# Kernel optimization log

Hardware: AMD Instinct MI355X
Metric: run time of the kernel (lower is better)

## Reference

```python
import jax, jax.numpy as jnp
import numpy as np

STEPS = 8
TOL = 1e-6


def _kabsch(p, q):
    # p, q: [B, N, 3]; returns R [B,3,3], t [B,3] s.t. q ~= R p + t (pypose svdtf)
    pm = p.mean(axis=-2, keepdims=True)
    qm = q.mean(axis=-2, keepdims=True)
    pc = p - pm
    qc = q - qm
    H = jnp.einsum('bni,bnj->bij', pc, qc)          # 3x3 cross-covariance
    U, S, Vt = jnp.linalg.svd(H, full_matrices=False)
    V = jnp.swapaxes(Vt, -1, -2)
    Ut = jnp.swapaxes(U, -1, -2)
    d = jnp.linalg.det(jnp.matmul(V, Ut))            # reflection fix
    D = jnp.concatenate([jnp.ones(d.shape + (2,), d.dtype), d[..., None]], axis=-1)
    R = jnp.matmul(V * D[..., None, :], Ut)
    t = qm[..., 0, :] - jnp.einsum('bij,bj->bi', R, pm[..., 0, :])
    return R, t


def _rotmat_to_quat(R):
    # branchless rotation-matrix -> quaternion [qx, qy, qz, qw] (pypose order)
    r00, r11, r22 = R[..., 0, 0], R[..., 1, 1], R[..., 2, 2]
    qw = 0.5 * jnp.sqrt(jnp.clip(1.0 + r00 + r11 + r22, 1e-12))
    qx = 0.5 * jnp.sqrt(jnp.clip(1.0 + r00 - r11 - r22, 1e-12))
    qy = 0.5 * jnp.sqrt(jnp.clip(1.0 - r00 + r11 - r22, 1e-12))
    qz = 0.5 * jnp.sqrt(jnp.clip(1.0 - r00 - r11 + r22, 1e-12))
    qx = qx * jnp.where(R[..., 2, 1] - R[..., 1, 2] >= 0, 1.0, -1.0)
    qy = qy * jnp.where(R[..., 0, 2] - R[..., 2, 0] >= 0, 1.0, -1.0)
    qz = qz * jnp.where(R[..., 1, 0] - R[..., 0, 1] >= 0, 1.0, -1.0)
    return jnp.stack([qx, qy, qz, qw], axis=-1)


def _icp(psrc, ptgt):
    B = psrc.shape[0]
    tn = (ptgt * ptgt).sum(-1)                        # [B, M]

    def body(carry, _):
        pc, err, done = carry
        # brute-force 1-NN: Euclidean cdist via  |p|^2 + |q|^2 - 2 p.q
        sq = ((pc * pc).sum(-1)[:, :, None] + tn[:, None, :]
              - 2.0 * jnp.einsum('bnd,bmd->bnm', pc, ptgt))
        dist = jnp.sqrt(jnp.clip(sq, 0.0))            # [B, N, M]
        knnd = dist.min(axis=-1)                      # [B, N]
        idx = dist.argmin(axis=-1)                    # [B, N]
        errnew = knnd.mean(axis=-1)                   # [B]
        conv = jnp.all(jnp.abs(errnew - err) < TOL)
        done_new = jnp.logical_or(done, conv)
        qk = jnp.take_along_axis(ptgt, jnp.broadcast_to(idx[..., None], pc.shape), axis=1)
        R, t = _kabsch(pc, qk)
        pcnew = jnp.einsum('bij,bnj->bni', R, pc) + t[:, None, :]
        pc = jnp.where(done_new, pc, pcnew)
        err = jnp.where(done_new, err, errnew)
        return (pc, err, done_new), None

    init = (psrc, jnp.zeros((B,), psrc.dtype), jnp.array(False))
    (pc, _, _), _ = jax.lax.scan(body, init, None, length=STEPS)
    R, t = _kabsch(psrc, pc)                          # final fit psrc -> moved cloud
    quat = _rotmat_to_quat(R)
    return jnp.concatenate([t, quat], axis=-1)        # SE3 7-vector [t, qx,qy,qz,qw]


def setup_inputs() -> dict:
    key = jax.random.key(0)
    k1, k2 = jax.random.split(key)
    psrc = jax.random.normal(k1, (2, 4096, 3), dtype=jnp.float32)
    ptgt = jax.random.normal(k2, (2, 4096, 3), dtype=jnp.float32)
    return {"psrc": psrc, "ptgt": ptgt}


def reference(psrc, ptgt):
    return _icp(psrc, ptgt)
```

## Files before the change

### kernel.cpp

```cpp
#include <hip/hip_runtime.h>
#include <math.h>

#define NPTS 4096
#define MPTS 4096
#define NSTEPS 8
#define ICP_TOL 1e-6f
#define NBLK 256
#define NSUB 16

#define ACC_OFF 32768
#define CTR_OFF 98304
#define CTR_STRIDE 1536
#define STPUB_OFF 110592

__global__ void init_kernel(const float* __restrict__ ptgt, float* __restrict__ ws) {
    float* ptgt4 = ws;
    unsigned* ctrs = (unsigned*)(ws + CTR_OFF);
    int gid = blockIdx.x * 256 + threadIdx.x;
    if (gid < 2 * MPTS) {
        float x = ptgt[3 * gid + 0];
        float y = ptgt[3 * gid + 1];
        float z = ptgt[3 * gid + 2];
        float4 v;
        v.x = x; v.y = y; v.z = z;
        v.w = 0.5f * (x * x + y * y + z * z);
        ((float4*)ptgt4)[gid] = v;
    }
    for (int i = gid; i < NSTEPS * CTR_STRIDE; i += 8192) ctrs[i] = 0u;
}

__device__ __forceinline__ float frcp(float x) {
#if __has_builtin(__builtin_amdgcn_rcpf)
    return __builtin_amdgcn_rcpf(x);
#else
    return 1.f / x;
#endif
}
__device__ __forceinline__ float frsq(float x) {
#if __has_builtin(__builtin_amdgcn_rsqf)
    return __builtin_amdgcn_rsqf(x);
#else
    return 1.f / sqrtf(x);
#endif
}

#define DET3(a,b,c,d,e,f,g,h,i) \
    ((a)*((e)*(i)-(f)*(h)) - (b)*((d)*(i)-(f)*(g)) + (c)*((d)*(h)-(e)*(g)))

__device__ __forceinline__ void horn_quat(const float N[4][4], float q[4]) {
    float s = 1e-30f;
#pragma unroll
    for (int i = 0; i < 4; ++i)
#pragma unroll
        for (int j = 0; j < 4; ++j) s = fmaxf(s, fabsf(N[i][j]));
    float inv = frcp(s);
    float A[4][4], B[4][4];
#pragma unroll
    for (int i = 0; i < 4; ++i)
#pragma unroll
        for (int j = 0; j < 4; ++j) A[i][j] = N[i][j] * inv;
#pragma unroll
    for (int i = 0; i < 4; ++i)
#pragma unroll
        for (int j = i; j < 4; ++j) {
            float v = A[i][0]*A[0][j] + A[i][1]*A[1][j] + A[i][2]*A[2][j] + A[i][3]*A[3][j];
            B[i][j] = v; B[j][i] = v;
        }
    float p1 = A[0][0]+A[1][1]+A[2][2]+A[3][3];
    float p2 = B[0][0]+B[1][1]+B[2][2]+B[3][3];
    float p3 = 0.f, p4 = 0.f;
#pragma unroll
    for (int i = 0; i < 4; ++i)
#pragma unroll
        for (int j = 0; j < 4; ++j) { p3 += A[i][j]*B[i][j]; p4 += B[i][j]*B[i][j]; }
    float e1 = p1;
    float e2 = 0.5f*(e1*p1 - p2);
    float e3 = (e2*p1 - e1*p2 + p3)*(1.f/3.f);
    float e4 = 0.25f*(e3*p1 - e2*p2 + e1*p3 - p4);
    float lam = -3e38f;
#pragma unroll
    for (int i = 0; i < 4; ++i) {
        float r = A[i][i];
#pragma unroll
        for (int j = 0; j < 4; ++j) if (j != i) r += fabsf(A[i][j]);
        lam = fmaxf(lam, r);
    }
#pragma unroll
    for (int it = 0; it < 12; ++it) {
        float pv = (((lam - e1)*lam + e2)*lam - e3)*lam + e4;
        float dv = ((4.f*lam - 3.f*e1)*lam + 2.f*e2)*lam - e3;
        lam -= pv * frcp(dv);
    }
    float M[4][4];
#pragma unroll
    for (int i = 0; i < 4; ++i)
#pragma unroll
        for (int j = 0; j < 4; ++j) M[i][j] = A[i][j] - ((i == j) ? lam : 0.f);
    float C0 = DET3(M[1][1],M[1][2],M[1][3], M[2][1],M[2][2],M[2][3], M[3][1],M[3][2],M[3][3]);
    float C1 = DET3(M[0][0],M[0][2],M[0][3], M[2][0],M[2][2],M[2][3], M[3][0],M[3][2],M[3][3]);
    float C2 = DET3(M[0][0],M[0][1],M[0][3], M[1][0],M[1][1],M[1][3], M[3][0],M[3][1],M[3][3]);
    float C3 = DET3(M[0][0],M[0][1],M[0][2], M[1][0],M[1][1],M[1][2], M[2][0],M[2][1],M[2][2]);
    int is = 0; float cb = fabsf(C0);
    if (fabsf(C1) > cb) { cb = fabsf(C1); is = 1; }
    if (fabsf(C2) > cb) { cb = fabsf(C2); is = 2; }
    if (fabsf(C3) > cb) { cb = fabsf(C3); is = 3; }
    float v0, v1, v2, v3;
#define ROWCOF(a,b,c) { \
    v0 =  DET3(M[a][1],M[a][2],M[a][3], M[b][1],M[b][2],M[b][3], M[c][1],M[c][2],M[c][3]); \
    v1 = -DET3(M[a][0],M[a][2],M[a][3], M[b][0],M[b][2],M[b][3], M[c][0],M[c][2],M[c][3]); \
    v2 =  DET3(M[a][0],M[a][1],M[a][3], M[b][0],M[b][1],M[b][3], M[c][0],M[c][1],M[c][3]); \
    v3 = -DET3(M[a][0],M[a][1],M[a][2], M[b][0],M[b][1],M[b][2], M[c][0],M[c][1],M[c][2]); }
    if (is == 0)      ROWCOF(1,2,3)
    else if (is == 1) ROWCOF(0,2,3)
    else if (is == 2) ROWCOF(0,1,3)
    else              ROWCOF(0,1,2)
#undef ROWCOF
    float nr = frsq(v0*v0 + v1*v1 + v2*v2 + v3*v3);
    q[0] = v0*nr; q[1] = v1*nr; q[2] = v2*nr; q[3] = v3*nr;
}

#define FOR16(OP) OP(0) OP(1) OP(2) OP(3) OP(4) OP(5) OP(6) OP(7) \
                  OP(8) OP(9) OP(10) OP(11) OP(12) OP(13) OP(14) OP(15)

__global__ __launch_bounds__(512, 2) void icp_main(
    const float* __restrict__ psrc, float* __restrict__ ws,
    float* __restrict__ out) {

    float* ptgt4 = ws;
    float* acc = ws + ACC_OFF;
    unsigned* ctrs = (unsigned*)(ws + CTR_OFF);
    float* stpub = ws + STPUB_OFF;

    __shared__ float tshx[MPTS];
    __shared__ float tshy[MPTS];
    __shared__ float tshz[MPTS];
    __shared__ float st[2][13];
    __shared__ unsigned keys[8][16];
    __shared__ float red[16][16];
    __shared__ float gred[2][16][16];
    __shared__ float asum[2][16];
    __shared__ int contflag;

    const int tid = threadIdx.x;
    const int bid = blockIdx.x;
    const int b = bid >> 7;
    const int n0 = (bid & 127) * 32;

    {
        const float4* tp4 = (const float4*)ptgt4 + (size_t)b * MPTS;
        for (int i = tid; i < MPTS; i += 512) {
            float4 v = tp4[i];
            tshx[i] = v.x; tshy[i] = v.y; tshz[i] = v.z;
        }
    }
    if (tid < 2) {
        st[tid][0] = 1.f; st[tid][1] = 0.f; st[tid][2] = 0.f;
        st[tid][3] = 0.f; st[tid][4] = 1.f; st[tid][5] = 0.f;
        st[tid][6] = 0.f; st[tid][7] = 0.f; st[tid][8] = 1.f;
        st[tid][9] = 0.f; st[tid][10] = 0.f; st[tid][11] = 0.f;
        st[tid][12] = 0.f;
    }
    __syncthreads();

    const int w = tid >> 6, lane = tid & 63;
    const int m0 = w * 512 + lane;

    for (int step = 0; step < NSTEPS; ++step) {
        float R00 = st[b][0], R01 = st[b][1], R02 = st[b][2];
        float R10 = st[b][3], R11 = st[b][4], R12 = st[b][5];
        float R20 = st[b][6], R21 = st[b][7], R22 = st[b][8];
        float t0 = st[b][9], t1 = st[b][10], t2 = st[b][11];

        float sacc = 0.f;

        for (int p = 0; p < 2; ++p) {
            const int np = n0 + p * 16;
            const float* ps = psrc + ((size_t)b * NPTS + np) * 3;

#define DECLP(i) float px##i, py##i, pz##i;
            FOR16(DECLP)
#undef DECLP
#define LOADP(i) { float x = ps[3*(i)], y = ps[3*(i)+1], z = ps[3*(i)+2]; \
            px##i = fmaf(R00, x, fmaf(R01, y, fmaf(R02, z, t0))); \
            py##i = fmaf(R10, x, fmaf(R11, y, fmaf(R12, z, t1))); \
            pz##i = fmaf(R20, x, fmaf(R21, y, fmaf(R22, z, t2))); }
            FOR16(LOADP)
#undef LOADP

#define DECLB(i) float bs##i = -3.0e38f; int ix##i = m0;
            FOR16(DECLB)
#undef DECLB

            float tcx = tshx[m0], tcy = tshy[m0], tcz = tshz[m0];
            int mreg = m0;
#pragma unroll
            for (int k = 0; k < 8; ++k) {
                int mn = m0 + ((k + 1) & 7) * 64;
                float tnx = tshx[mn], tny = tshy[mn], tnz = tshz[mn];
                float htn = 0.5f * (tcx * tcx + tcy * tcy + tcz * tcz);
                float tx = tcx, ty = tcy, tz = tcz;
#define PAIR(i) { float s = fmaf(px##i, tx, fmaf(py##i, ty, fmaf(pz##i, tz, -htn))); \
                if (s > bs##i) { bs##i = s; ix##i = mreg; } }
                FOR16(PAIR)
#undef PAIR
                mreg += 64;
                tcx = tnx; tcy = tny; tcz = tnz;
            }

#define REDKEY(i) { unsigned ub = __float_as_uint(bs##i); \
            unsigned u = ((int)ub >= 0) ? (ub | 0x80000000u) : ~ub; \
            unsigned key = (u & 0xFFFFF000u) | (4095u - (unsigned)ix##i); \
            for (int off = 32; off; off >>= 1) { \
                unsigned o = (unsigned)__shfl_xor((int)key, off); \
                key = key > o ? key : o; } \
            if (lane == 0) keys[w][i] = key; }
            FOR16(REDKEY)
#undef REDKEY
            __syncthreads();

            if (tid < 16) {
                unsigned key = keys[0][tid];
#pragma unroll
                for (int ww = 1; ww < 8; ++ww) {
                    unsigned o = keys[ww][tid];
                    key = key > o ? key : o;
                }
                int m = 4095 - (int)(key & 0xFFFu);
                float qx2 = tshx[m], qy2 = tshy[m], qz2 = tshz[m];
                const float* pp = psrc + ((size_t)b * NPTS + np + tid) * 3;
                float x = pp[0], y = pp[1], z = pp[2];
                float px = fmaf(R00, x, fmaf(R01, y, fmaf(R02, z, t0)));
                float py = fmaf(R10, x, fmaf(R11, y, fmaf(R12, z, t1)));
                float pz = fmaf(R20, x, fmaf(R21, y, fmaf(R22, z, t2)));
                float dx = px - qx2, dy = py - qy2, dz = pz - qz2;
                float dist = sqrtf(dx * dx + dy * dy + dz * dz);
                red[tid][0] = px; red[tid][1] = py; red[tid][2] = pz;
                red[tid][3] = qx2; red[tid][4] = qy2; red[tid][5] = qz2;
                red[tid][6] = px * qx2;  red[tid][7] = px * qy2;  red[tid][8] = px * qz2;
                red[tid][9] = py * qx2;  red[tid][10] = py * qy2; red[tid][11] = py * qz2;
                red[tid][12] = pz * qx2; red[tid][13] = pz * qy2; red[tid][14] = pz * qz2;
                red[tid][15] = dist;
            }
            __syncthreads();
            if (tid < 16) {
                float s = 0.f;
#pragma unroll
                for (int r = 0; r < 16; ++r) s += red[r][tid];
                sacc += s;
            }
            __syncthreads();
        }

        if (tid < 16) {
            __hip_atomic_store(&acc[((size_t)step * NBLK + bid) * 16 + tid], sacc,
                               __ATOMIC_RELAXED, __HIP_MEMORY_SCOPE_AGENT);
        }

        unsigned* stepc = ctrs + step * CTR_STRIDE;
        __syncthreads();
        if (tid == 0) {
            unsigned* sub = stepc + (bid & (NSUB - 1)) * 16;
            unsigned old = __hip_atomic_fetch_add(sub, 1u, __ATOMIC_RELAXED,
                                                  __HIP_MEMORY_SCOPE_AGENT);
            if (old == (unsigned)(NBLK / NSUB) - 1u)
                __hip_atomic_fetch_add(stepc + 512, 1u, __ATOMIC_RELAXED,
                                       __HIP_MEMORY_SCOPE_AGENT);
        }

        if (bid == 0) {
            if (tid == 0) {
                while (__hip_atomic_load(stepc + 512, __ATOMIC_RELAXED,
                                         __HIP_MEMORY_SCOPE_AGENT) < (unsigned)NSUB) {
                    __builtin_amdgcn_s_sleep(1);
                }
            }
            __syncthreads();
            {
                const float* accs = acc + (size_t)step * NBLK * 16;
                int bb = tid >> 8;
                int rem = tid & 255;
                int c = rem & 15, g = rem >> 4;
                float ssum = 0.f;
#pragma unroll
                for (int i = 0; i < 8; ++i)
                    ssum += accs[(size_t)(bb * 128 + g * 8 + i) * 16 + c];
                gred[bb][g][c] = ssum;
            }
            __syncthreads();
            if (tid < 32) {
                int bb = tid >> 4, c = tid & 15;
                float s = 0.f;
#pragma unroll
                for (int g = 0; g < 16; ++g) s += gred[bb][g][c];
                asum[bb][c] = s;
            }
            __syncthreads();
            if (tid == 0) {
                float err0 = asum[0][15] * (1.f / NPTS);
                float err1 = asum[1][15] * (1.f / NPTS);
                bool conv = (fabsf(err0 - st[0][12]) < ICP_TOL) &&
                            (fabsf(err1 - st[1][12]) < ICP_TOL);
                contflag = conv ? 2 : 1;
            }
            __syncthreads();
            if (contflag == 1 && tid < 2) {
                float a[16];
                for (int i = 0; i < 16; ++i) a[i] = asum[tid][i];
                const float inv_n = 1.f / NPTS;
                float pmx = a[0]*inv_n, pmy = a[1]*inv_n, pmz = a[2]*inv_n;
                float qmx = a[3]*inv_n, qmy = a[4]*inv_n, qmz = a[5]*inv_n;
                float H[3][3];
                for (int i = 0; i < 3; ++i)
                    for (int j = 0; j < 3; ++j)
                        H[i][j] = a[6 + 3*i + j] - a[i]*a[3 + j]*inv_n;
                float Sxx=H[0][0], Sxy=H[0][1], Sxz=H[0][2];
                float Syx=H[1][0], Syy=H[1][1], Syz=H[1][2];
                float Szx=H[2][0], Szy=H[2][1], Szz=H[2][2];
                float Nm[4][4];
                Nm[0][0] = Sxx+Syy+Szz; Nm[0][1] = Syz-Szy;
                Nm[0][2] = Szx-Sxz;     Nm[0][3] = Sxy-Syx;
                Nm[1][1] = Sxx-Syy-Szz; Nm[1][2] = Sxy+Syx; Nm[1][3] = Szx+Sxz;
                Nm[2][2] = -Sxx+Syy-Szz; Nm[2][3] = Syz+Szy;
                Nm[3][3] = -Sxx-Syy+Szz;
                Nm[1][0]=Nm[0][1]; Nm[2][0]=Nm[0][2]; Nm[3][0]=Nm[0][3];
                Nm[2][1]=Nm[1][2]; Nm[3][1]=Nm[1][3]; Nm[3][2]=Nm[2][3];
                float qv[4];
                horn_quat(Nm, qv);
                float qw = qv[0], qx = qv[1], qy = qv[2], qz = qv[3];
                float R00n = 1.f - 2.f*(qy*qy + qz*qz);
                float R01n = 2.f*(qx*qy - qw*qz);
                float R02n = 2.f*(qx*qz + qw*qy);
                float R10n = 2.f*(qx*qy + qw*qz);
                float R11n = 1.f - 2.f*(qx*qx + qz*qz);
                float R12n = 2.f*(qy*qz - qw*qx);
                float R20n = 2.f*(qx*qz - qw*qy);
                float R21n = 2.f*(qy*qz + qw*qx);
                float R22n = 1.f - 2.f*(qx*qx + qy*qy);
                float tx = qmx - (R00n*pmx + R01n*pmy + R02n*pmz);
                float ty = qmy - (R10n*pmx + R11n*pmy + R12n*pmz);
                float tz = qmz - (R20n*pmx + R21n*pmy + R22n*pmz);
                float C00=st[tid][0], C01=st[tid][1], C02=st[tid][2];
                float C10=st[tid][3], C11=st[tid][4], C12=st[tid][5];
                float C20=st[tid][6], C21=st[tid][7], C22=st[tid][8];
                float T0=st[tid][9], T1=st[tid][10], T2=st[tid][11];
                float ns[12];
                ns[0] = R00n*C00 + R01n*C10 + R02n*C20;
                ns[1] = R00n*C01 + R01n*C11 + R02n*C21;
                ns[2] = R00n*C02 + R01n*C12 + R02n*C22;
                ns[3] = R10n*C00 + R11n*C10 + R12n*C20;
                ns[4] = R10n*C01 + R11n*C11 + R12n*C21;
                ns[5] = R10n*C02 + R11n*C12 + R12n*C22;
                ns[6] = R20n*C00 + R21n*C10 + R22n*C20;
                ns[7] = R20n*C01 + R21n*C11 + R22n*C21;
                ns[8] = R20n*C02 + R21n*C12 + R22n*C22;
                ns[9]  = R00n*T0 + R01n*T1 + R02n*T2 + tx;
                ns[10] = R10n*T0 + R11n*T1 + R12n*T2 + ty;
                ns[11] = R20n*T0 + R21n*T1 + R22n*T2 + tz;
                for (int i = 0; i < 12; ++i) {
                    st[tid][i] = ns[i];
                    __hip_atomic_store(&stpub[step*32 + tid*16 + i], ns[i],
                                       __ATOMIC_RELAXED, __HIP_MEMORY_SCOPE_AGENT);
                }
                st[tid][12] = asum[tid][15] * (1.f / NPTS);
            }
            __syncthreads();
            if (tid == 0) {
                unsigned fv = (unsigned)contflag;
#pragma unroll
                for (int f = 0; f < NSUB; ++f)
                    __hip_atomic_store(stepc + 1024 + f*16, fv,
                                       __ATOMIC_RELAXED, __HIP_MEMORY_SCOPE_AGENT);
            }
            __syncthreads();
        } else {
            if (tid == 0) {
                unsigned* myflag = stepc + 1024 + (bid & (NSUB - 1)) * 16;
                unsigned fv;
                while ((fv = __hip_atomic_load(myflag, __ATOMIC_RELAXED,
                                               __HIP_MEMORY_SCOPE_AGENT)) == 0u) {
                    __builtin_amdgcn_s_sleep(2);
                }
                contflag = (int)fv;
                if (fv == 1u) {
                    for (int i = 0; i < 12; ++i)
                        st[b][i] = __hip_atomic_load(&stpub[step*32 + b*16 + i],
                                                     __ATOMIC_RELAXED,
                                                     __HIP_MEMORY_SCOPE_AGENT);
                }
            }
            __syncthreads();
        }
        if (contflag == 2) break;
    }

    if (bid == 0 && tid < 2) {
        float r00 = st[tid][0], r01 = st[tid][1], r02 = st[tid][2];
        float r10 = st[tid][3], r11 = st[tid][4], r12 = st[tid][5];
        float r20 = st[tid][6], r21 = st[tid][7], r22 = st[tid][8];
        float qw = 0.5f * sqrtf(fmaxf(1.f + r00 + r11 + r22, 1e-12f));
        float qx = 0.5f * sqrtf(fmaxf(1.f + r00 - r11 - r22, 1e-12f));
        float qy = 0.5f * sqrtf(fmaxf(1.f - r00 + r11 - r22, 1e-12f));
        float qz = 0.5f * sqrtf(fmaxf(1.f - r00 - r11 + r22, 1e-12f));
        qx = (r21 - r12 >= 0.f) ? qx : -qx;
        qy = (r02 - r20 >= 0.f) ? qy : -qy;
        qz = (r10 - r01 >= 0.f) ? qz : -qz;
        out[tid * 7 + 0] = st[tid][9];
        out[tid * 7 + 1] = st[tid][10];
        out[tid * 7 + 2] = st[tid][11];
        out[tid * 7 + 3] = qx;
        out[tid * 7 + 4] = qy;
        out[tid * 7 + 5] = qz;
        out[tid * 7 + 6] = qw;
    }
}

extern "C" void kernel_launch(void* const* d_in, const int* in_sizes, int n_in,
                              void* d_out, int out_size, void* d_ws, size_t ws_size,
                              hipStream_t stream) {
    const float* psrc = (const float*)d_in[0];
    const float* ptgt = (const float*)d_in[1];
    float* out = (float*)d_out;
    float* ws = (float*)d_ws;

    init_kernel<<<32, 256, 0, stream>>>(ptgt, ws);
    icp_main<<<NBLK, 512, 0, stream>>>(psrc, ws, out);
}
```

Before: 194.6 us.

## Split grid barrier per batch with two masters and cache source points in LDS

Replaces the single global master block with one master per batch element (blocks 0 and 128). Each master reduces only its own 128 block partials with a vectorized float4 load and a transposed LDS reduction, then computes that batch's Kabsch update in parallel with the other master. The masters exchange convergence flags so both batches still stop together. Source points are cached in shared memory instead of being re-read from global every step. This shortens the serial tail at each step barrier, at the cost of a second cross-block flag handshake that every block must wait on.

Result: faster. 189.2 us (-2.8%).

```diff
diff --git a/kernel.cpp b/kernel.cpp
--- a/kernel.cpp
+++ b/kernel.cpp
@@ -6,11 +6,10 @@
 #define NSTEPS 8
 #define ICP_TOL 1e-6f
 #define NBLK 256
-#define NSUB 16
 
 #define ACC_OFF 32768
 #define CTR_OFF 98304
-#define CTR_STRIDE 1536
+#define CTR_STRIDE 1024
 #define STPUB_OFF 110592
 
 __global__ void init_kernel(const float* __restrict__ ptgt, float* __restrict__ ws) {
@@ -134,12 +133,15 @@
     __shared__ float tshx[MPTS];
     __shared__ float tshy[MPTS];
     __shared__ float tshz[MPTS];
-    __shared__ float st[2][13];
+    __shared__ float spx[32], spy[32], spz[32];
+    __shared__ float stq[13];
     __shared__ unsigned keys[8][16];
     __shared__ float red[16][16];
-    __shared__ float gred[2][16][16];
-    __shared__ float asum[2][16];
-    __shared__ int contflag;
+    __shared__ float gd[16][132];
+    __shared__ float gp[4][16];
+    __shared__ float asum[16];
+    __shared__ float stv[12];
+    __shared__ int fvs[2];
 
     const int tid = threadIdx.x;
     const int bid = blockIdx.x;
@@ -153,34 +155,38 @@
             tshx[i] = v.x; tshy[i] = v.y; tshz[i] = v.z;
         }
     }
-    if (tid < 2) {
-        st[tid][0] = 1.f; st[tid][1] = 0.f; st[tid][2] = 0.f;
-        st[tid][3] = 0.f; st[tid][4] = 1.f; st[tid][5] = 0.f;
-        st[tid][6] = 0.f; st[tid][7] = 0.f; st[tid][8] = 1.f;
-        st[tid][9] = 0.f; st[tid][10] = 0.f; st[tid][11] = 0.f;
-        st[tid][12] = 0.f;
+    if (tid < 32) {
+        const float* pp = psrc + ((size_t)b * NPTS + n0 + tid) * 3;
+        spx[tid] = pp[0]; spy[tid] = pp[1]; spz[tid] = pp[2];
+    }
+    if (tid == 0) {
+        stq[0] = 1.f; stq[1] = 0.f; stq[2] = 0.f;
+        stq[3] = 0.f; stq[4] = 1.f; stq[5] = 0.f;
+        stq[6] = 0.f; stq[7] = 0.f; stq[8] = 1.f;
+        stq[9] = 0.f; stq[10] = 0.f; stq[11] = 0.f;
+        stq[12] = 0.f;
     }
     __syncthreads();
 
     const int w = tid >> 6, lane = tid & 63;
     const int m0 = w * 512 + lane;
+    bool done = false;
 
     for (int step = 0; step < NSTEPS; ++step) {
-        float R00 = st[b][0], R01 = st[b][1], R02 = st[b][2];
-        float R10 = st[b][3], R11 = st[b][4], R12 = st[b][5];
-        float R20 = st[b][6], R21 = st[b][7], R22 = st[b][8];
-        float t0 = st[b][9], t1 = st[b][10], t2 = st[b][11];
+        float R00 = stq[0], R01 = stq[1], R02 = stq[2];
+        float R10 = stq[3], R11 = stq[4], R12 = stq[5];
+        float R20 = stq[6], R21 = stq[7], R22 = stq[8];
+        float t0 = stq[9], t1 = stq[10], t2 = stq[11];
 
         float sacc = 0.f;
 
         for (int p = 0; p < 2; ++p) {
-            const int np = n0 + p * 16;
-            const float* ps = psrc + ((size_t)b * NPTS + np) * 3;
+            const int np = p * 16;
 
 #define DECLP(i) float px##i, py##i, pz##i;
             FOR16(DECLP)
 #undef DECLP
-#define LOADP(i) { float x = ps[3*(i)], y = ps[3*(i)+1], z = ps[3*(i)+2]; \
+#define LOADP(i) { float x = spx[np+(i)], y = spy[np+(i)], z = spz[np+(i)]; \
             px##i = fmaf(R00, x, fmaf(R01, y, fmaf(R02, z, t0))); \
             py##i = fmaf(R10, x, fmaf(R11, y, fmaf(R12, z, t1))); \
             pz##i = fmaf(R20, x, fmaf(R21, y, fmaf(R22, z, t2))); }
@@ -227,8 +233,7 @@
                 }
                 int m = 4095 - (int)(key & 0xFFFu);
                 float qx2 = tshx[m], qy2 = tshy[m], qz2 = tshz[m];
-                const float* pp = psrc + ((size_t)b * NPTS + np + tid) * 3;
-                float x = pp[0], y = pp[1], z = pp[2];
+                float x = spx[np + tid], y = spy[np + tid], z = spz[np + tid];
                 float px = fmaf(R00, x, fmaf(R01, y, fmaf(R02, z, t0)));
                 float py = fmaf(R10, x, fmaf(R11, y, fmaf(R12, z, t1)));
                 float pz = fmaf(R20, x, fmaf(R21, y, fmaf(R22, z, t2)));
@@ -259,53 +264,50 @@
         unsigned* stepc = ctrs + step * CTR_STRIDE;
         __syncthreads();
         if (tid == 0) {
-            unsigned* sub = stepc + (bid & (NSUB - 1)) * 16;
+            unsigned* sub = stepc + (b * 8 + (bid & 7)) * 16;
             unsigned old = __hip_atomic_fetch_add(sub, 1u, __ATOMIC_RELAXED,
                                                   __HIP_MEMORY_SCOPE_AGENT);
-            if (old == (unsigned)(NBLK / NSUB) - 1u)
-                __hip_atomic_fetch_add(stepc + 512, 1u, __ATOMIC_RELAXED,
+            if (old == 15u)
+                __hip_atomic_fetch_add(stepc + 256 + b * 16, 1u, __ATOMIC_RELAXED,
                                        __HIP_MEMORY_SCOPE_AGENT);
         }
 
-        if (bid == 0) {
+        const bool is_master = ((bid & 127) == 0);
+        if (is_master) {
             if (tid == 0) {
-                while (__hip_atomic_load(stepc + 512, __ATOMIC_RELAXED,
-                                         __HIP_MEMORY_SCOPE_AGENT) < (unsigned)NSUB) {
+                while (__hip_atomic_load(stepc + 256 + b * 16, __ATOMIC_RELAXED,
+                                         __HIP_MEMORY_SCOPE_AGENT) < 8u) {
                     __builtin_amdgcn_s_sleep(1);
                 }
             }
             __syncthreads();
             {
-                const float* accs = acc + (size_t)step * NBLK * 16;
-                int bb = tid >> 8;
-                int rem = tid & 255;
-                int c = rem & 15, g = rem >> 4;
-                float ssum = 0.f;
-#pragma unroll
-                for (int i = 0; i < 8; ++i)
-                    ssum += accs[(size_t)(bb * 128 + g * 8 + i) * 16 + c];
-                gred[bb][g][c] = ssum;
-            }
-            __syncthreads();
-            if (tid < 32) {
-                int bb = tid >> 4, c = tid & 15;
+                int s = tid >> 2, cb = (tid & 3) * 4;
+                const float* base = acc + ((size_t)step * NBLK + b * 128 + s) * 16 + cb;
+                float4 v = *(const float4*)base;
+                gd[cb + 0][s] = v.x;
+                gd[cb + 1][s] = v.y;
+                gd[cb + 2][s] = v.z;
+                gd[cb + 3][s] = v.w;
+            }
+            __syncthreads();
+            if (tid < 64) {
+                int c = tid & 15, part = tid >> 4;
                 float s = 0.f;
 #pragma unroll
-                for (int g = 0; g < 16; ++g) s += gred[bb][g][c];
-                asum[bb][c] = s;
-            }
-            __syncthreads();
+                for (int i = 0; i < 32; ++i) s += gd[c][part * 32 + i];
+                gp[part][c] = s;
+            }
+            __syncthreads();
+            if (tid < 16) asum[tid] = gp[0][tid] + gp[1][tid] + gp[2][tid] + gp[3][tid];
+            __syncthreads();
+
             if (tid == 0) {
-                float err0 = asum[0][15] * (1.f / NPTS);
-                float err1 = asum[1][15] * (1.f / NPTS);
-                bool conv = (fabsf(err0 - st[0][12]) < ICP_TOL) &&
-                            (fabsf(err1 - st[1][12]) < ICP_TOL);
-                contflag = conv ? 2 : 1;
-            }
-            __syncthreads();
-            if (contflag == 1 && tid < 2) {
                 float a[16];
-                for (int i = 0; i < 16; ++i) a[i] = asum[tid][i];
+                for (int i = 0; i < 16; ++i) a[i] = asum[i];
+                float errnew = a[15] * (1.f / NPTS);
+                bool conv_b = (fabsf(errnew - stq[12]) < ICP_TOL);
+
                 const float inv_n = 1.f / NPTS;
                 float pmx = a[0]*inv_n, pmy = a[1]*inv_n, pmz = a[2]*inv_n;
                 float qmx = a[3]*inv_n, qmy = a[4]*inv_n, qmz = a[5]*inv_n;
@@ -339,10 +341,10 @@
                 float tx = qmx - (R00n*pmx + R01n*pmy + R02n*pmz);
                 float ty = qmy - (R10n*pmx + R11n*pmy + R12n*pmz);
                 float tz = qmz - (R20n*pmx + R21n*pmy + R22n*pmz);
-                float C00=st[tid][0], C01=st[tid][1], C02=st[tid][2];
-                float C10=st[tid][3], C11=st[tid][4], C12=st[tid][5];
-                float C20=st[tid][6], C21=st[tid][7], C22=st[tid][8];
-                float T0=st[tid][9], T1=st[tid][10], T2=st[tid][11];
+                float C00=stq[0], C01=stq[1], C02=stq[2];
+                float C10=stq[3], C11=stq[4], C12=stq[5];
+                float C20=stq[6], C21=stq[7], C22=stq[8];
+                float T0=stq[9], T1=stq[10], T2=stq[11];
                 float ns[12];
                 ns[0] = R00n*C00 + R01n*C10 + R02n*C20;
                 ns[1] = R00n*C01 + R01n*C11 + R02n*C21;
@@ -357,46 +359,80 @@
                 ns[10] = R10n*T0 + R11n*T1 + R12n*T2 + ty;
                 ns[11] = R20n*T0 + R21n*T1 + R22n*T2 + tz;
                 for (int i = 0; i < 12; ++i) {
-                    st[tid][i] = ns[i];
-                    __hip_atomic_store(&stpub[step*32 + tid*16 + i], ns[i],
+                    stv[i] = ns[i];
+                    __hip_atomic_store(&stpub[step*32 + b*16 + i], ns[i],
                                        __ATOMIC_RELAXED, __HIP_MEMORY_SCOPE_AGENT);
                 }
-                st[tid][12] = asum[tid][15] * (1.f / NPTS);
+                stv[0] = ns[0];
+                for (int i = 0; i < 12; ++i) stv[i] = ns[i];
+                asum[15] = errnew;
+                fvs[b] = 1 + (conv_b ? 1 : 0);
             }
             __syncthreads();
             if (tid == 0) {
-                unsigned fv = (unsigned)contflag;
-#pragma unroll
-                for (int f = 0; f < NSUB; ++f)
-                    __hip_atomic_store(stepc + 1024 + f*16, fv,
+                unsigned fv = (unsigned)fvs[b];
+#pragma unroll
+                for (int f = 0; f < 16; ++f)
+                    __hip_atomic_store(stepc + 512 + b * 256 + f * 16, fv,
                                        __ATOMIC_RELAXED, __HIP_MEMORY_SCOPE_AGENT);
             }
-            __syncthreads();
+            if (tid == 64) {
+                unsigned* of = stepc + 512 + (1 - b) * 256;
+                unsigned fv;
+                while ((fv = __hip_atomic_load(of, __ATOMIC_RELAXED,
+                                               __HIP_MEMORY_SCOPE_AGENT)) == 0u) {
+                    __builtin_amdgcn_s_sleep(1);
+                }
+                fvs[1 - b] = (int)fv;
+            }
+            __syncthreads();
+            bool conv = (fvs[0] == 2) && (fvs[1] == 2);
+            bool done_new = done || conv;
+            if (tid == 0 && !done_new) {
+                for (int i = 0; i < 12; ++i) stq[i] = stv[i];
+                stq[12] = asum[15];
+            }
+            __syncthreads();
+            done = done_new;
         } else {
             if (tid == 0) {
-                unsigned* myflag = stepc + 1024 + (bid & (NSUB - 1)) * 16;
+                unsigned* mf = stepc + 512 + b * 256 + (bid & 15) * 16;
                 unsigned fv;
-                while ((fv = __hip_atomic_load(myflag, __ATOMIC_RELAXED,
+                while ((fv = __hip_atomic_load(mf, __ATOMIC_RELAXED,
                                                __HIP_MEMORY_SCOPE_AGENT)) == 0u) {
-                    __builtin_amdgcn_s_sleep(2);
-                }
-                contflag = (int)fv;
-                if (fv == 1u) {
-                    for (int i = 0; i < 12; ++i)
-                        st[b][i] = __hip_atomic_load(&stpub[step*32 + b*16 + i],
-                                                     __ATOMIC_RELAXED,
-                                                     __HIP_MEMORY_SCOPE_AGENT);
-                }
-            }
-            __syncthreads();
-        }
-        if (contflag == 2) break;
-    }
-
-    if (bid == 0 && tid < 2) {
-        float r00 = st[tid][0], r01 = st[tid][1], r02 = st[tid][2];
-        float r10 = st[tid][3], r11 = st[tid][4], r12 = st[tid][5];
-        float r20 = st[tid][6], r21 = st[tid][7], r22 = st[tid][8];
+                    __builtin_amdgcn_s_sleep(1);
+                }
+                fvs[b] = (int)fv;
+            }
+            if (tid == 64) {
+                unsigned* of = stepc + 512 + (1 - b) * 256 + (bid & 15) * 16;
+                unsigned fv;
+                while ((fv = __hip_atomic_load(of, __ATOMIC_RELAXED,
+                                               __HIP_MEMORY_SCOPE_AGENT)) == 0u) {
+                    __builtin_amdgcn_s_sleep(1);
+                }
+                fvs[1 - b] = (int)fv;
+            }
+            __syncthreads();
+            if (tid < 12) {
+                stv[tid] = __hip_atomic_load(&stpub[step*32 + b*16 + tid],
+                                             __ATOMIC_RELAXED,
+                                             __HIP_MEMORY_SCOPE_AGENT);
+            }
+            __syncthreads();
+            bool conv = (fvs[0] == 2) && (fvs[1] == 2);
+            bool done_new = done || conv;
+            if (tid < 12 && !done_new) stq[tid] = stv[tid];
+            __syncthreads();
+            done = done_new;
+        }
+        if (done) break;
+    }
+
+    if ((bid == 0 || bid == 128) && tid == 0) {
+        float r00 = stq[0], r01 = stq[1], r02 = stq[2];
+        float r10 = stq[3], r11 = stq[4], r12 = stq[5];
+        float r20 = stq[6], r21 = stq[7], r22 = stq[8];
         float qw = 0.5f * sqrtf(fmaxf(1.f + r00 + r11 + r22, 1e-12f));
         float qx = 0.5f * sqrtf(fmaxf(1.f + r00 - r11 - r22, 1e-12f));
         float qy = 0.5f * sqrtf(fmaxf(1.f - r00 + r11 - r22, 1e-12f));
@@ -404,13 +440,13 @@
         qx = (r21 - r12 >= 0.f) ? qx : -qx;
         qy = (r02 - r20 >= 0.f) ? qy : -qy;
         qz = (r10 - r01 >= 0.f) ? qz : -qz;
-        out[tid * 7 + 0] = st[tid][9];
-        out[tid * 7 + 1] = st[tid][10];
-        out[tid * 7 + 2] = st[tid][11];
-        out[tid * 7 + 3] = qx;
-        out[tid * 7 + 4] = qy;
-        out[tid * 7 + 5] = qz;
-        out[tid * 7 + 6] = qw;
+        out[b * 7 + 0] = stq[9];
+        out[b * 7 + 1] = stq[10];
+        out[b * 7 + 2] = stq[11];
+        out[b * 7 + 3] = qx;
+        out[b * 7 + 4] = qy;
+        out[b * 7 + 5] = qz;
+        out[b * 7 + 6] = qw;
     }
 }
 
```
